# Optimization experiments

Measured on AMD Instinct MI355X. Metric: run time of the kernel, lower is better.

Reference implementation:

```python
import jax, jax.numpy as jnp
import numpy as np
import math

EPS = 1e-6  # PCEN eps


def _logit(p):
    return math.log(p / (1.0 - p))


def _pcen(mel, log_s, log_alpha, log_delta, log_r, dmin, dmax):
    """PCEN: per-channel energy normalization. mel: (B, M, T); params: (M,)."""
    s = jnp.clip(jax.nn.sigmoid(log_s), 0.05, 0.3)            # (M,)
    alpha = jnp.clip(jax.nn.sigmoid(log_alpha), 0.9, 0.999)   # (M,)
    delta = jnp.clip(jnp.exp(log_delta), dmin, dmax)          # (M,)
    r = jnp.clip(jax.nn.sigmoid(log_r), 0.05, 0.25)           # (M,)

    # IIR smoother over time: smoother_0 = mel[..., 0];
    # for t in 0..T-1: smoother = (1-s)*smoother + s*mel_t  (t=0 included -> smoothed_0 = mel_0)
    mel_t = jnp.transpose(mel, (2, 0, 1))  # (T, B, M)

    def step(sm, x):
        sm = (1.0 - s) * sm + s * x
        return sm, sm

    _, smoothed_t = jax.lax.scan(step, mel_t[0], mel_t)
    smoothed = jnp.transpose(smoothed_t, (1, 2, 0))  # (B, M, T)

    gain = (EPS + smoothed) ** (-alpha[None, :, None])
    d = delta[None, :, None]
    rr = r[None, :, None]
    return (mel * gain + d) ** rr - d ** rr


def setup_inputs() -> dict:
    key = jax.random.key(0)
    B, M, T = 64, 80, 4000
    mel = jax.random.uniform(key, (B, M, T), dtype=jnp.float32)
    f = jnp.full
    return {
        "mel": mel,
        # non-stationary expert PCEN (s=0.025, alpha=0.99, delta=2.0, r=0.5)
        "log_s_ns": f((M,), _logit(0.025), jnp.float32),
        "log_alpha_ns": f((M,), _logit(0.99), jnp.float32),
        "log_delta_ns": f((M,), math.log(2.0), jnp.float32),
        "log_r_ns": f((M,), _logit(0.5), jnp.float32),
        # stationary expert PCEN (s=0.15, alpha=0.99, delta=0.01, r=0.1)
        "log_s_st": f((M,), _logit(0.15), jnp.float32),
        "log_alpha_st": f((M,), _logit(0.99), jnp.float32),
        "log_delta_st": f((M,), math.log(0.01), jnp.float32),
        "log_r_st": f((M,), _logit(0.1), jnp.float32),
        "gate_temp": jnp.asarray(5.0, jnp.float32),
    }


def reference(mel, log_s_ns, log_alpha_ns, log_delta_ns, log_r_ns,
              log_s_st, log_alpha_st, log_delta_st, log_r_st, gate_temp):
    out_ns = _pcen(mel, log_s_ns, log_alpha_ns, log_delta_ns, log_r_ns, 0.5, 5.0)
    out_st = _pcen(mel, log_s_st, log_alpha_st, log_delta_st, log_r_st, 0.001, 0.1)

    # routing signal: spectral flatness + spectral tilt (0 learnable params)
    log_mel = jnp.log(mel + 1e-8)
    geo = jnp.exp(jnp.mean(log_mel, axis=1, keepdims=True))          # (B,1,T)
    arith = jnp.mean(mel, axis=1, keepdims=True) + 1e-8
    sf = jnp.clip(geo / arith, 0.0, 1.0)

    M = mel.shape[1]
    low = jnp.mean(mel[:, : M // 3, :], axis=1, keepdims=True)
    high = jnp.mean(mel[:, 2 * M // 3 :, :], axis=1, keepdims=True)
    tilt = jnp.clip(low / (low + high + 1e-8), 0.0, 1.0)

    sf_adj = sf + (1.0 - sf) * jax.nn.relu(tilt - 0.6)
    gate = jax.nn.sigmoid(gate_temp * (sf_adj - 0.5))
    return gate * out_st + (1.0 - gate) * out_ns
```

## Files before the change

### kernel.cpp

```cpp
#include <hip/hip_runtime.h>
#include <math.h>

static constexpr int kM = 80;
static constexpr int kT = 4000;
static constexpr int kB = 64;
static constexpr int kLow = kM / 3;
static constexpr int kHighStart = 2 * kM / 3;
static constexpr int kHighCount = kM - kHighStart;
#define EPSF 1e-6f
#define LOG2E 1.4426950408889634f

typedef float vfloat4 __attribute__((ext_vector_type(4)));
typedef float vfloat2 __attribute__((ext_vector_type(2)));

__device__ __forceinline__ float hw_exp2(float x) { return __builtin_amdgcn_exp2f(x); }
__device__ __forceinline__ float hw_log2(float x) { return __builtin_amdgcn_logf(x); }

__device__ __forceinline__ float fast_sigmoid(float x) {
    return __builtin_amdgcn_rcpf(1.0f + hw_exp2(-x * LOG2E));
}

__global__ __launch_bounds__(256) void gate_kernel(
    const float* __restrict__ mel,
    const float* __restrict__ gate_temp,
    float* __restrict__ gate)
{
    const int lane = threadIdx.x & 63;
    const int wid  = threadIdx.x >> 6;
    const int b    = blockIdx.y;
    const int t0   = blockIdx.x * 256 + lane * 4;
    const bool valid = (t0 < kT);

    const float* base = mel + (size_t)b * kM * kT + t0;

    vfloat4 slog = {0.f,0.f,0.f,0.f}, ssum = {0.f,0.f,0.f,0.f};
    vfloat4 slow = {0.f,0.f,0.f,0.f}, shigh = {0.f,0.f,0.f,0.f};

    const int m0 = wid * 20;
    if (valid) {
        #pragma unroll
        for (int j = 0; j < 20; ++j) {
            const int m = m0 + j;
            const vfloat4 v = *reinterpret_cast<const vfloat4*>(base + (size_t)m * kT);
            vfloat4 lg;
            lg.x = hw_log2(v.x + 1e-8f); lg.y = hw_log2(v.y + 1e-8f);
            lg.z = hw_log2(v.z + 1e-8f); lg.w = hw_log2(v.w + 1e-8f);
            slog += lg;
            ssum += v;
            if (m < kLow)        slow  += v;
            if (m >= kHighStart) shigh += v;
        }
    }

    __shared__ vfloat4 sh[4][4][64];
    sh[wid][0][lane] = slog;
    sh[wid][1][lane] = ssum;
    sh[wid][2][lane] = slow;
    sh[wid][3][lane] = shigh;
    __syncthreads();

    if (wid == 0 && valid) {
        slog  = sh[0][0][lane] + sh[1][0][lane] + sh[2][0][lane] + sh[3][0][lane];
        ssum  = sh[0][1][lane] + sh[1][1][lane] + sh[2][1][lane] + sh[3][1][lane];
        slow  = sh[0][2][lane] + sh[1][2][lane] + sh[2][2][lane] + sh[3][2][lane];
        shigh = sh[0][3][lane] + sh[1][3][lane] + sh[2][3][lane] + sh[3][3][lane];

        const float gt = gate_temp[0];
        float sl[4]  = {slog.x, slog.y, slog.z, slog.w};
        float ss[4]  = {ssum.x, ssum.y, ssum.z, ssum.w};
        float lo[4]  = {slow.x, slow.y, slow.z, slow.w};
        float hi[4]  = {shigh.x, shigh.y, shigh.z, shigh.w};
        float g4[4];
        #pragma unroll
        for (int q = 0; q < 4; ++q) {
            const float geo   = hw_exp2(sl[q] * (1.0f / kM));
            const float arith = ss[q] * (1.0f / kM) + 1e-8f;
            float sf = geo * __builtin_amdgcn_rcpf(arith);
            sf = fminf(fmaxf(sf, 0.0f), 1.0f);
            const float low  = lo[q] * (1.0f / kLow);
            const float high = hi[q] * (1.0f / kHighCount);
            float tilt = low * __builtin_amdgcn_rcpf(low + high + 1e-8f);
            tilt = fminf(fmaxf(tilt, 0.0f), 1.0f);
            const float sfa = sf + (1.0f - sf) * fmaxf(tilt - 0.6f, 0.0f);
            g4[q] = fast_sigmoid(gt * (sfa - 0.5f));
        }
        vfloat4 o; o.x = g4[0]; o.y = g4[1]; o.z = g4[2]; o.w = g4[3];
        *reinterpret_cast<vfloat4*>(gate + (size_t)b * kT + t0) = o;
    }
}

__global__ __launch_bounds__(256, 4) void pcen_kernel(
    const float* __restrict__ mel,
    const float* __restrict__ ls_ns, const float* __restrict__ la_ns,
    const float* __restrict__ ld_ns, const float* __restrict__ lr_ns,
    const float* __restrict__ ls_st, const float* __restrict__ la_st,
    const float* __restrict__ ld_st, const float* __restrict__ lr_st,
    const float* __restrict__ gate,
    float* __restrict__ out)
{
    const int m = blockIdx.x;
    const int b = blockIdx.y;

    const float s_ns     = fminf(fmaxf(fast_sigmoid(ls_ns[m]), 0.05f), 0.3f);
    const float alpha_ns = fminf(fmaxf(fast_sigmoid(la_ns[m]), 0.9f), 0.999f);
    const float delta_ns = fminf(fmaxf(hw_exp2(ld_ns[m] * LOG2E), 0.5f), 5.0f);
    const float r_ns     = fminf(fmaxf(fast_sigmoid(lr_ns[m]), 0.05f), 0.25f);
    const float s_st     = fminf(fmaxf(fast_sigmoid(ls_st[m]), 0.05f), 0.3f);
    const float alpha_st = fminf(fmaxf(fast_sigmoid(la_st[m]), 0.9f), 0.999f);
    const float delta_st = fminf(fmaxf(hw_exp2(ld_st[m] * LOG2E), 0.001f), 0.1f);
    const float r_st     = fminf(fmaxf(fast_sigmoid(lr_st[m]), 0.05f), 0.25f);
    const float dr_ns = hw_exp2(r_ns * hw_log2(delta_ns));
    const float dr_st = hw_exp2(r_st * hw_log2(delta_st));

    const vfloat2 a2 = {1.0f - s_ns, 1.0f - s_st};
    const vfloat2 s2 = {s_ns, s_st};
    const vfloat2 d2 = {delta_ns, delta_st};
    const float man = -alpha_ns, mas = -alpha_st;

    const size_t rowoff = ((size_t)b * kM + m) * kT;
    const float* row = mel + rowoff;

    const int tid = threadIdx.x;
    const int t0  = tid * 16;
    const bool valid = (t0 < kT);

    float x[16];
    float gv[16];
    if (valid) {
        const float4* p = reinterpret_cast<const float4*>(row + t0);
        #pragma unroll
        for (int q = 0; q < 4; ++q) {
            const float4 v = p[q];
            x[4*q+0] = v.x; x[4*q+1] = v.y; x[4*q+2] = v.z; x[4*q+3] = v.w;
        }
        const float4* gp = reinterpret_cast<const float4*>(gate + (size_t)b * kT + t0);
        #pragma unroll
        for (int q = 0; q < 4; ++q) {
            const float4 v = gp[q];
            gv[4*q+0] = v.x; gv[4*q+1] = v.y; gv[4*q+2] = v.z; gv[4*q+3] = v.w;
        }
    } else {
        #pragma unroll
        for (int k = 0; k < 16; ++k) { x[k] = 0.0f; gv[k] = 0.0f; }
    }

    __shared__ float sv0;
    if (tid == 0) sv0 = x[0];

    vfloat2 Av = {1.0f, 1.0f}, Bv = {0.0f, 0.0f};
    if (valid) {
        #pragma unroll
        for (int k = 0; k < 16; ++k) {
            Bv = a2 * Bv + s2 * x[k];
        }
        const vfloat2 p2 = a2 * a2;
        const vfloat2 p4 = p2 * p2;
        const vfloat2 p8 = p4 * p4;
        Av = p8 * p8;
    }

    const int lane = tid & 63;
    const int wid  = tid >> 6;

    #pragma unroll
    for (int d = 1; d < 64; d <<= 1) {
        const float qAn = __shfl_up(Av.x, d);
        const float qAs = __shfl_up(Av.y, d);
        const float qBn = __shfl_up(Bv.x, d);
        const float qBs = __shfl_up(Bv.y, d);
        if (lane >= d) {
            const vfloat2 qA = {qAn, qAs};
            const vfloat2 qB = {qBn, qBs};
            Bv = Av * qB + Bv;
            Av = Av * qA;
        }
    }

    __shared__ vfloat2 wA[4], wB[4];
    if (lane == 63) { wA[wid] = Av; wB[wid] = Bv; }
    __syncthreads();

    vfloat2 eA, eB;
    eA.x = __shfl_up(Av.x, 1); eA.y = __shfl_up(Av.y, 1);
    eB.x = __shfl_up(Bv.x, 1); eB.y = __shfl_up(Bv.y, 1);
    if (lane == 0) { eA = (vfloat2){1.0f, 1.0f}; eB = (vfloat2){0.0f, 0.0f}; }

    vfloat2 pA = {1.0f, 1.0f}, pB = {0.0f, 0.0f};
    for (int j = 0; j < wid; ++j) {
        pB = wA[j] * pB + wB[j];
        pA = wA[j] * pA;
    }

    const vfloat2 v0 = {sv0, sv0};
    vfloat2 sm = eA * (pA * v0 + pB) + eB;

    if (valid) {
        float4* op = reinterpret_cast<float4*>(out + rowoff + t0);
        #pragma unroll
        for (int q = 0; q < 4; ++q) {
            float4 v;
            #pragma unroll
            for (int j = 0; j < 4; ++j) {
                const int k = 4*q + j;
                const float xv = x[k];
                sm = a2 * sm + s2 * xv;
                vfloat2 g2;
                g2.x = hw_exp2(man * hw_log2(sm.x + EPSF));
                g2.y = hw_exp2(mas * hw_log2(sm.y + EPSF));
                const vfloat2 u2 = g2 * xv + d2;
                const float on = hw_exp2(r_ns * hw_log2(u2.x)) - dr_ns;
                const float os = hw_exp2(r_st * hw_log2(u2.y)) - dr_st;
                (&v.x)[j] = fmaf(gv[k], os - on, on);
            }
            op[q] = v;
        }
    }
}

extern "C" void kernel_launch(void* const* d_in, const int* in_sizes, int n_in,
                              void* d_out, int out_size, void* d_ws, size_t ws_size,
                              hipStream_t stream)
{
    const float* mel       = (const float*)d_in[0];
    const float* ls_ns     = (const float*)d_in[1];
    const float* la_ns     = (const float*)d_in[2];
    const float* ld_ns     = (const float*)d_in[3];
    const float* lr_ns     = (const float*)d_in[4];
    const float* ls_st     = (const float*)d_in[5];
    const float* la_st     = (const float*)d_in[6];
    const float* ld_st     = (const float*)d_in[7];
    const float* lr_st     = (const float*)d_in[8];
    const float* gate_temp = (const float*)d_in[9];
    float* out  = (float*)d_out;
    float* gate = (float*)d_ws;

    dim3 gA(16, kB);
    gate_kernel<<<gA, 256, 0, stream>>>(mel, gate_temp, gate);

    dim3 gB(kM, kB);
    pcen_kernel<<<gB, 256, 0, stream>>>(mel, ls_ns, la_ns, ld_ns, lr_ns,
                                        ls_st, la_st, ld_st, lr_st, gate, out);
}
```

Baseline: 182.5 us.

## Map PCEN threads to rows with time chunks and truncated IIR warm-up

The PCEN kernel now gives each thread one (batch, mel) row and one 160-sample time chunk, instead of running a 256-thread block per row with a wave-level shuffle scan. Each chunk rebuilds its starting smoother state by rerunning the recurrence over the previous 256 samples, split into four partial sums combined with powers of (1-s). Chunk 1 replays from t=0 exactly. This removes the shuffle scan, shared-memory sync and idle lanes, but reads extra mel data for warm-up. Neighbouring lanes now read different rows, so loads are strided and uncoalesced, and the grid shrinks to 500 blocks. Truncating the warm-up is a small approximation that the clamp s ≥ 0.05 keeps tiny.

```diff
diff --git a/kernel.cpp b/kernel.cpp
--- a/kernel.cpp
+++ b/kernel.cpp
@@ -7,6 +7,9 @@
 static constexpr int kLow = kM / 3;
 static constexpr int kHighStart = 2 * kM / 3;
 static constexpr int kHighCount = kM - kHighStart;
+static constexpr int kChunks = 25;
+static constexpr int kChunkLen = kT / kChunks;
+static constexpr int kWarm = 256;
 #define EPSF 1e-6f
 #define LOG2E 1.4426950408889634f
 
@@ -89,7 +92,7 @@
     }
 }
 
-__global__ __launch_bounds__(256, 4) void pcen_kernel(
+__global__ __launch_bounds__(256) void pcen_kernel(
     const float* __restrict__ mel,
     const float* __restrict__ ls_ns, const float* __restrict__ la_ns,
     const float* __restrict__ ld_ns, const float* __restrict__ lr_ns,
@@ -98,8 +101,10 @@
     const float* __restrict__ gate,
     float* __restrict__ out)
 {
-    const int m = blockIdx.x;
-    const int b = blockIdx.y;
+    const int row = blockIdx.x * 256 + threadIdx.x;
+    const int c   = blockIdx.y;
+    const int b   = row / kM;
+    const int m   = row - b * kM;
 
     const float s_ns     = fminf(fmaxf(fast_sigmoid(ls_ns[m]), 0.05f), 0.3f);
     const float alpha_ns = fminf(fmaxf(fast_sigmoid(la_ns[m]), 0.9f), 0.999f);
@@ -117,103 +122,73 @@
     const vfloat2 d2 = {delta_ns, delta_st};
     const float man = -alpha_ns, mas = -alpha_st;
 
-    const size_t rowoff = ((size_t)b * kM + m) * kT;
-    const float* row = mel + rowoff;
-
-    const int tid = threadIdx.x;
-    const int t0  = tid * 16;
-    const bool valid = (t0 < kT);
-
-    float x[16];
-    float gv[16];
-    if (valid) {
-        const float4* p = reinterpret_cast<const float4*>(row + t0);
+    const size_t rowoff = (size_t)row * kT;
+    const float* rowp = mel + rowoff;
+    const int t0 = c * kChunkLen;
+
+    vfloat2 sm = {0.0f, 0.0f};
+    if (c == 0) {
+        const float x0 = rowp[0];
+        sm.x = x0; sm.y = x0;
+    } else {
+        if (c == 1) {
+            const float x0 = rowp[0];
+            sm.x = x0; sm.y = x0;
+        }
+        const int tw = (c == 1) ? 0 : (t0 - kWarm);
+        const int nw = (c == 1) ? (kChunkLen / 16) : (kWarm / 16);
+        const float4* wp = reinterpret_cast<const float4*>(rowp + tw);
+
+        vfloat2 B0 = {0,0}, B1 = {0,0}, B2 = {0,0}, B3 = {0,0};
+        #pragma unroll 2
+        for (int i = 0; i < nw; ++i) {
+            const float4 v0 = wp[i];
+            const float4 v1 = wp[nw + i];
+            const float4 v2 = wp[2*nw + i];
+            const float4 v3 = wp[3*nw + i];
+            B0 = a2 * B0 + s2 * v0.x; B0 = a2 * B0 + s2 * v0.y;
+            B0 = a2 * B0 + s2 * v0.z; B0 = a2 * B0 + s2 * v0.w;
+            B1 = a2 * B1 + s2 * v1.x; B1 = a2 * B1 + s2 * v1.y;
+            B1 = a2 * B1 + s2 * v1.z; B1 = a2 * B1 + s2 * v1.w;
+            B2 = a2 * B2 + s2 * v2.x; B2 = a2 * B2 + s2 * v2.y;
+            B2 = a2 * B2 + s2 * v2.z; B2 = a2 * B2 + s2 * v2.w;
+            B3 = a2 * B3 + s2 * v3.x; B3 = a2 * B3 + s2 * v3.y;
+            B3 = a2 * B3 + s2 * v3.z; B3 = a2 * B3 + s2 * v3.w;
+        }
+        const vfloat2 p2  = a2  * a2;
+        const vfloat2 p4  = p2  * p2;
+        const vfloat2 p8  = p4  * p4;
+        const vfloat2 p16 = p8  * p8;
+        const vfloat2 p32 = p16 * p16;
+        const vfloat2 p64 = p32 * p32;
+        const vfloat2 ps  = (c == 1) ? (p32 * p8) : p64;
+        const vfloat2 ps2 = ps * ps;
+        const vfloat2 ps4 = ps2 * ps2;
+        sm = ps4 * sm + (((B0 * ps + B1) * ps + B2) * ps + B3);
+    }
+
+    const float4* xp = reinterpret_cast<const float4*>(rowp + t0);
+    const float4* gp = reinterpret_cast<const float4*>(gate + (size_t)b * kT + t0);
+    float4* op = reinterpret_cast<float4*>(out + rowoff + t0);
+
+    #pragma unroll 4
+    for (int i = 0; i < kChunkLen / 4; ++i) {
+        const float4 xv = xp[i];
+        const float4 gg = gp[i];
+        float4 o;
         #pragma unroll
-        for (int q = 0; q < 4; ++q) {
-            const float4 v = p[q];
-            x[4*q+0] = v.x; x[4*q+1] = v.y; x[4*q+2] = v.z; x[4*q+3] = v.w;
-        }
-        const float4* gp = reinterpret_cast<const float4*>(gate + (size_t)b * kT + t0);
-        #pragma unroll
-        for (int q = 0; q < 4; ++q) {
-            const float4 v = gp[q];
-            gv[4*q+0] = v.x; gv[4*q+1] = v.y; gv[4*q+2] = v.z; gv[4*q+3] = v.w;
-        }
-    } else {
-        #pragma unroll
-        for (int k = 0; k < 16; ++k) { x[k] = 0.0f; gv[k] = 0.0f; }
-    }
-
-    __shared__ float sv0;
-    if (tid == 0) sv0 = x[0];
-
-    vfloat2 Av = {1.0f, 1.0f}, Bv = {0.0f, 0.0f};
-    if (valid) {
-        #pragma unroll
-        for (int k = 0; k < 16; ++k) {
-            Bv = a2 * Bv + s2 * x[k];
-        }
-        const vfloat2 p2 = a2 * a2;
-        const vfloat2 p4 = p2 * p2;
-        const vfloat2 p8 = p4 * p4;
-        Av = p8 * p8;
-    }
-
-    const int lane = tid & 63;
-    const int wid  = tid >> 6;
-
-    #pragma unroll
-    for (int d = 1; d < 64; d <<= 1) {
-        const float qAn = __shfl_up(Av.x, d);
-        const float qAs = __shfl_up(Av.y, d);
-        const float qBn = __shfl_up(Bv.x, d);
-        const float qBs = __shfl_up(Bv.y, d);
-        if (lane >= d) {
-            const vfloat2 qA = {qAn, qAs};
-            const vfloat2 qB = {qBn, qBs};
-            Bv = Av * qB + Bv;
-            Av = Av * qA;
-        }
-    }
-
-    __shared__ vfloat2 wA[4], wB[4];
-    if (lane == 63) { wA[wid] = Av; wB[wid] = Bv; }
-    __syncthreads();
-
-    vfloat2 eA, eB;
-    eA.x = __shfl_up(Av.x, 1); eA.y = __shfl_up(Av.y, 1);
-    eB.x = __shfl_up(Bv.x, 1); eB.y = __shfl_up(Bv.y, 1);
-    if (lane == 0) { eA = (vfloat2){1.0f, 1.0f}; eB = (vfloat2){0.0f, 0.0f}; }
-
-    vfloat2 pA = {1.0f, 1.0f}, pB = {0.0f, 0.0f};
-    for (int j = 0; j < wid; ++j) {
-        pB = wA[j] * pB + wB[j];
-        pA = wA[j] * pA;
-    }
-
-    const vfloat2 v0 = {sv0, sv0};
-    vfloat2 sm = eA * (pA * v0 + pB) + eB;
-
-    if (valid) {
-        float4* op = reinterpret_cast<float4*>(out + rowoff + t0);
-        #pragma unroll
-        for (int q = 0; q < 4; ++q) {
-            float4 v;
-            #pragma unroll
-            for (int j = 0; j < 4; ++j) {
-                const int k = 4*q + j;
-                const float xv = x[k];
-                sm = a2 * sm + s2 * xv;
-                vfloat2 g2;
-                g2.x = hw_exp2(man * hw_log2(sm.x + EPSF));
-                g2.y = hw_exp2(mas * hw_log2(sm.y + EPSF));
-                const vfloat2 u2 = g2 * xv + d2;
-                const float on = hw_exp2(r_ns * hw_log2(u2.x)) - dr_ns;
-                const float os = hw_exp2(r_st * hw_log2(u2.y)) - dr_st;
-                (&v.x)[j] = fmaf(gv[k], os - on, on);
-            }
-            op[q] = v;
-        }
+        for (int j = 0; j < 4; ++j) {
+            const float x1 = (&xv.x)[j];
+            sm = a2 * sm + s2 * x1;
+            vfloat2 g2;
+            g2.x = hw_exp2(man * hw_log2(sm.x + EPSF));
+            g2.y = hw_exp2(mas * hw_log2(sm.y + EPSF));
+            const vfloat2 u2 = g2 * x1 + d2;
+            const float on = hw_exp2(r_ns * hw_log2(u2.x)) - dr_ns;
+            const float os = hw_exp2(r_st * hw_log2(u2.y)) - dr_st;
+            (&o.x)[j] = fmaf((&gg.x)[j], os - on, on);
+        }
+        op[i] = o;
     }
 }
 
@@ -237,7 +212,7 @@
     dim3 gA(16, kB);
     gate_kernel<<<gA, 256, 0, stream>>>(mel, gate_temp, gate);
 
-    dim3 gB(kM, kB);
+    dim3 gB(kB * kM / 256, kChunks);
     pcen_kernel<<<gB, 256, 0, stream>>>(mel, ls_ns, la_ns, ld_ns, lr_ns,
                                         ls_st, la_st, ld_st, lr_st, gate, out);
 }
```

Result: slower. 245.0 us (+34.2%).

## Replace exact IIR scan with truncated warm-up recurrence from LDS

Applied to the files above, without the earlier changes.

The PCEN kernel drops the exact parallel prefix scan (wave shuffles plus cross-wave combine) and instead stages each row in skewed LDS. Each thread recomputes its starting smoother state from only the previous 192 samples, split into four 48-sample chains combined with powers of (1-s). This assumes (1-s)^192 is negligible, which holds only because s is clamped to at least 0.05, so the result is a truncation approximation. The gate kernel is also reworked so each thread reduces two columns over all 80 mel bins, with no cross-wave LDS reduction.

```diff
diff --git a/kernel.cpp b/kernel.cpp
--- a/kernel.cpp
+++ b/kernel.cpp
@@ -7,6 +7,8 @@
 static constexpr int kLow = kM / 3;
 static constexpr int kHighStart = 2 * kM / 3;
 static constexpr int kHighCount = kM - kHighStart;
+static constexpr int kWarm = 192;
+static constexpr int kLdsWords = kT + kT / 16;
 #define EPSF 1e-6f
 #define LOG2E 1.4426950408889634f
 
@@ -19,77 +21,59 @@
 __device__ __forceinline__ float fast_sigmoid(float x) {
     return __builtin_amdgcn_rcpf(1.0f + hw_exp2(-x * LOG2E));
 }
+
+__device__ __forceinline__ int skw(int w) { return w + (w >> 4); }
 
 __global__ __launch_bounds__(256) void gate_kernel(
     const float* __restrict__ mel,
     const float* __restrict__ gate_temp,
     float* __restrict__ gate)
 {
-    const int lane = threadIdx.x & 63;
-    const int wid  = threadIdx.x >> 6;
-    const int b    = blockIdx.y;
-    const int t0   = blockIdx.x * 256 + lane * 4;
-    const bool valid = (t0 < kT);
-
-    const float* base = mel + (size_t)b * kM * kT + t0;
-
-    vfloat4 slog = {0.f,0.f,0.f,0.f}, ssum = {0.f,0.f,0.f,0.f};
-    vfloat4 slow = {0.f,0.f,0.f,0.f}, shigh = {0.f,0.f,0.f,0.f};
-
-    const int m0 = wid * 20;
-    if (valid) {
-        #pragma unroll
-        for (int j = 0; j < 20; ++j) {
-            const int m = m0 + j;
-            const vfloat4 v = *reinterpret_cast<const vfloat4*>(base + (size_t)m * kT);
-            vfloat4 lg;
-            lg.x = hw_log2(v.x + 1e-8f); lg.y = hw_log2(v.y + 1e-8f);
-            lg.z = hw_log2(v.z + 1e-8f); lg.w = hw_log2(v.w + 1e-8f);
-            slog += lg;
-            ssum += v;
-            if (m < kLow)        slow  += v;
-            if (m >= kHighStart) shigh += v;
-        }
-    }
-
-    __shared__ vfloat4 sh[4][4][64];
-    sh[wid][0][lane] = slog;
-    sh[wid][1][lane] = ssum;
-    sh[wid][2][lane] = slow;
-    sh[wid][3][lane] = shigh;
-    __syncthreads();
-
-    if (wid == 0 && valid) {
-        slog  = sh[0][0][lane] + sh[1][0][lane] + sh[2][0][lane] + sh[3][0][lane];
-        ssum  = sh[0][1][lane] + sh[1][1][lane] + sh[2][1][lane] + sh[3][1][lane];
-        slow  = sh[0][2][lane] + sh[1][2][lane] + sh[2][2][lane] + sh[3][2][lane];
-        shigh = sh[0][3][lane] + sh[1][3][lane] + sh[2][3][lane] + sh[3][3][lane];
-
-        const float gt = gate_temp[0];
-        float sl[4]  = {slog.x, slog.y, slog.z, slog.w};
-        float ss[4]  = {ssum.x, ssum.y, ssum.z, ssum.w};
-        float lo[4]  = {slow.x, slow.y, slow.z, slow.w};
-        float hi[4]  = {shigh.x, shigh.y, shigh.z, shigh.w};
-        float g4[4];
-        #pragma unroll
-        for (int q = 0; q < 4; ++q) {
-            const float geo   = hw_exp2(sl[q] * (1.0f / kM));
-            const float arith = ss[q] * (1.0f / kM) + 1e-8f;
-            float sf = geo * __builtin_amdgcn_rcpf(arith);
-            sf = fminf(fmaxf(sf, 0.0f), 1.0f);
-            const float low  = lo[q] * (1.0f / kLow);
-            const float high = hi[q] * (1.0f / kHighCount);
-            float tilt = low * __builtin_amdgcn_rcpf(low + high + 1e-8f);
-            tilt = fminf(fmaxf(tilt, 0.0f), 1.0f);
-            const float sfa = sf + (1.0f - sf) * fmaxf(tilt - 0.6f, 0.0f);
-            g4[q] = fast_sigmoid(gt * (sfa - 0.5f));
-        }
-        vfloat4 o; o.x = g4[0]; o.y = g4[1]; o.z = g4[2]; o.w = g4[3];
-        *reinterpret_cast<vfloat4*>(gate + (size_t)b * kT + t0) = o;
-    }
-}
-
-__global__ __launch_bounds__(256, 4) void pcen_kernel(
+    const int b  = blockIdx.y;
+    const int tc = blockIdx.x * 256 + threadIdx.x;
+    if (tc >= kT / 2) return;
+
+    const float* base = mel + (size_t)b * kM * kT + (size_t)tc * 2;
+
+    vfloat2 slog = {0.f, 0.f}, ssum = {0.f, 0.f};
+    vfloat2 slow = {0.f, 0.f}, shigh = {0.f, 0.f};
+
+    #pragma unroll 16
+    for (int m = 0; m < kM; ++m) {
+        const vfloat2 v = *reinterpret_cast<const vfloat2*>(base + (size_t)m * kT);
+        vfloat2 lg;
+        lg.x = hw_log2(v.x + 1e-8f);
+        lg.y = hw_log2(v.y + 1e-8f);
+        slog += lg;
+        ssum += v;
+        if (m < kLow)        slow  += v;
+        if (m >= kHighStart) shigh += v;
+    }
+
+    const float gt = gate_temp[0];
+    vfloat2 o;
+    #pragma unroll
+    for (int q = 0; q < 2; ++q) {
+        const float sl = (q == 0) ? slog.x : slog.y;
+        const float ss = (q == 0) ? ssum.x : ssum.y;
+        const float lo = (q == 0) ? slow.x : slow.y;
+        const float hi = (q == 0) ? shigh.x : shigh.y;
+        const float geo   = hw_exp2(sl * (1.0f / kM));
+        const float arith = ss * (1.0f / kM) + 1e-8f;
+        float sf = geo * __builtin_amdgcn_rcpf(arith);
+        sf = fminf(fmaxf(sf, 0.0f), 1.0f);
+        const float low  = lo * (1.0f / kLow);
+        const float high = hi * (1.0f / kHighCount);
+        float tilt = low * __builtin_amdgcn_rcpf(low + high + 1e-8f);
+        tilt = fminf(fmaxf(tilt, 0.0f), 1.0f);
+        const float sfa = sf + (1.0f - sf) * fmaxf(tilt - 0.6f, 0.0f);
+        const float g = fast_sigmoid(gt * (sfa - 0.5f));
+        if (q == 0) o.x = g; else o.y = g;
+    }
+    *reinterpret_cast<vfloat2*>(gate + (size_t)b * kT + (size_t)tc * 2) = o;
+}
+
+__global__ __launch_bounds__(256) void pcen_kernel(
     const float* __restrict__ mel,
     const float* __restrict__ ls_ns, const float* __restrict__ la_ns,
     const float* __restrict__ ld_ns, const float* __restrict__ lr_ns,
@@ -124,6 +108,8 @@
     const int t0  = tid * 16;
     const bool valid = (t0 < kT);
 
+    __shared__ float xs[kLdsWords];
+
     float x[16];
     float gv[16];
     if (valid) {
@@ -139,60 +125,45 @@
             const float4 v = gp[q];
             gv[4*q+0] = v.x; gv[4*q+1] = v.y; gv[4*q+2] = v.z; gv[4*q+3] = v.w;
         }
-    } else {
-        #pragma unroll
-        for (int k = 0; k < 16; ++k) { x[k] = 0.0f; gv[k] = 0.0f; }
-    }
-
-    __shared__ float sv0;
-    if (tid == 0) sv0 = x[0];
-
-    vfloat2 Av = {1.0f, 1.0f}, Bv = {0.0f, 0.0f};
+        #pragma unroll
+        for (int k = 0; k < 16; ++k) xs[skw(t0 + k)] = x[k];
+    }
+    __syncthreads();
+
+    vfloat2 sm = {0.0f, 0.0f};
     if (valid) {
-        #pragma unroll
-        for (int k = 0; k < 16; ++k) {
-            Bv = a2 * Bv + s2 * x[k];
-        }
-        const vfloat2 p2 = a2 * a2;
-        const vfloat2 p4 = p2 * p2;
-        const vfloat2 p8 = p4 * p4;
-        Av = p8 * p8;
-    }
-
-    const int lane = tid & 63;
-    const int wid  = tid >> 6;
-
-    #pragma unroll
-    for (int d = 1; d < 64; d <<= 1) {
-        const float qAn = __shfl_up(Av.x, d);
-        const float qAs = __shfl_up(Av.y, d);
-        const float qBn = __shfl_up(Bv.x, d);
-        const float qBs = __shfl_up(Bv.y, d);
-        if (lane >= d) {
-            const vfloat2 qA = {qAn, qAs};
-            const vfloat2 qB = {qBn, qBs};
-            Bv = Av * qB + Bv;
-            Av = Av * qA;
-        }
-    }
-
-    __shared__ vfloat2 wA[4], wB[4];
-    if (lane == 63) { wA[wid] = Av; wB[wid] = Bv; }
-    __syncthreads();
-
-    vfloat2 eA, eB;
-    eA.x = __shfl_up(Av.x, 1); eA.y = __shfl_up(Av.y, 1);
-    eB.x = __shfl_up(Bv.x, 1); eB.y = __shfl_up(Bv.y, 1);
-    if (lane == 0) { eA = (vfloat2){1.0f, 1.0f}; eB = (vfloat2){0.0f, 0.0f}; }
-
-    vfloat2 pA = {1.0f, 1.0f}, pB = {0.0f, 0.0f};
-    for (int j = 0; j < wid; ++j) {
-        pB = wA[j] * pB + wB[j];
-        pA = wA[j] * pA;
-    }
-
-    const vfloat2 v0 = {sv0, sv0};
-    vfloat2 sm = eA * (pA * v0 + pB) + eB;
+        if (t0 >= kWarm) {
+            const int ws = t0 - kWarm;
+            vfloat2 B0 = {0,0}, B1 = {0,0}, B2 = {0,0}, B3 = {0,0};
+            #pragma unroll 4
+            for (int j = 0; j < 48; ++j) {
+                const float v0 = xs[skw(ws +   0 + j)];
+                const float v1 = xs[skw(ws +  48 + j)];
+                const float v2 = xs[skw(ws +  96 + j)];
+                const float v3 = xs[skw(ws + 144 + j)];
+                B0 = a2 * B0 + s2 * v0;
+                B1 = a2 * B1 + s2 * v1;
+                B2 = a2 * B2 + s2 * v2;
+                B3 = a2 * B3 + s2 * v3;
+            }
+            const vfloat2 p2  = a2  * a2;
+            const vfloat2 p4  = p2  * p2;
+            const vfloat2 p8  = p4  * p4;
+            const vfloat2 p16 = p8  * p8;
+            const vfloat2 p32 = p16 * p16;
+            const vfloat2 p48 = p32 * p16;
+            sm = ((B0 * p48 + B1) * p48 + B2) * p48 + B3;
+        } else if (t0 > 0) {
+            const float x0 = xs[0];
+            sm.x = x0; sm.y = x0;
+            for (int j = 0; j < t0; ++j) {
+                const float v = xs[skw(j)];
+                sm = a2 * sm + s2 * v;
+            }
+        } else {
+            sm.x = x[0]; sm.y = x[0];
+        }
+    }
 
     if (valid) {
         float4* op = reinterpret_cast<float4*>(out + rowoff + t0);
@@ -234,7 +205,7 @@
     float* out  = (float*)d_out;
     float* gate = (float*)d_ws;
 
-    dim3 gA(16, kB);
+    dim3 gA((kT / 2 + 255) / 256, kB);
     gate_kernel<<<gA, 256, 0, stream>>>(mel, gate_temp, gate);
 
     dim3 gB(kM, kB);
```

Measured after the change: 220.1 us. 1.21x slower.
